# Kernel optimization log

Measured on AMD Instinct MI355X. Metric: run time of the kernel, lower is better.

The kernel has to match this reference:

```python
import jax, jax.numpy as jnp
import numpy as np

# AWLoss config (matches init_kwargs): method='fft', filter_dim=2, filter_scale=2,
# mode='reverse', reduction='sum', epsilon=1e-9 (pre-whitening), std=1e-4, eta=0, gamma=0
EPSILON = 1e-9
STD = 1e-4
DIMS = (-2, -1)          # self.dims for filter_dim=2
FS = (3, 511, 511)       # get_filter_shape([B,3,256,256]): [nc, 2H-1, 2W-1]


def pad_signal(x, shape):
    # center-pad dims 1.. of x up to `shape` (extra sample on the right).
    pads = [(0, 0)]
    for i, s in enumerate(shape):
        p1 = (s - x.shape[i + 1]) // 2
        pads.append((p1, s - x.shape[i + 1] - p1))
    return jnp.pad(x, pads)


def make_penalty(shape, std):
    # inverted multivariate gaussian on [-1,1]^d grid: 0 at center, ->1 away
    axes = [jnp.linspace(-1.0, 1.0, n) for n in shape]
    mesh = jnp.stack(jnp.meshgrid(*axes, indexing='ij'), axis=-1)  # (h, w, 2)
    d = mesh.shape[-1]
    logp = -0.5 * jnp.sum((mesh / std) ** 2, axis=-1) \
           - 0.5 * d * jnp.log(2.0 * jnp.pi * std * std)
    rv = jnp.exp(logp)
    rv = rv / jnp.max(jnp.abs(rv))
    return -rv + jnp.max(rv)  # eta=0 => no random additive term


def wienerfft(x, y, fs, prwh):
    # least-squares Wiener filter transforming x into y, via FFT
    Fx_flip = jnp.fft.fftn(jnp.flip(x, DIMS), axes=DIMS)
    Fccorr = Fx_flip * jnp.fft.fftn(y, axes=DIMS)   # cross-correlation spectrum
    Facorr = Fx_flip * jnp.fft.fftn(x, axes=DIMS)   # auto-correlation spectrum
    Fdconv = (Fccorr + prwh) / (Facorr + prwh)      # regularized deconvolution
    # irfftn crops last axis to fs[-1]//2+1 (numpy/torch semantics match)
    rolled = jnp.fft.irfftn(Fdconv, s=fs[-2:], axes=DIMS)
    # roll: int(-n/2)-1 per trailing dim (n odd => -(n//2)-1)
    shifts = tuple(-(x.shape[i] // 2) - 1 for i in range(1, x.ndim))[-2:]
    return jnp.roll(rolled, shifts, axis=DIMS)


def awloss(recon, target):
    fs = FS
    recon_p = pad_signal(recon, fs)   # [B, C, 511, 511]
    target_p = pad_signal(target, fs)
    # mode='reverse': filter transforms target into recon
    x, y = target_p, recon_p
    v = wienerfft(x, y, fs, EPSILON)                       # [B, C, 511, 511]
    vnorm = jnp.sqrt(jnp.sum(v * v, axis=DIMS, keepdims=True))
    v = v / vnorm                                          # unit-energy filter
    T = make_penalty(fs[-2:], STD)                         # (511, 511)
    f = 0.5 * jnp.sum((T * v) ** 2)                        # reduction='sum'
    return f


def setup_inputs() -> dict:
    key = jax.random.key(0)
    k1, k2 = jax.random.split(key)
    recon = jax.random.normal(k1, (16, 3, 256, 256), dtype=jnp.float32)
    target = jax.random.normal(k2, (16, 3, 256, 256), dtype=jnp.float32)
    return {"recon": recon, "target": target}


def reference(recon, target):
    return awloss(recon, target)
```

## Files before the change

### kernel.cpp

```cpp
#include <hip/hip_runtime.h>
#include <math.h>


#define NCH 48
#define PADOFF 127
#define TWO_PI_F 6.283185307179586f

typedef float f32x4 __attribute__((ext_vector_type(4)));
typedef short s16x8 __attribute__((ext_vector_type(8)));
typedef unsigned short u16;

typedef __attribute__((address_space(1))) const unsigned char* gas_p;
typedef __attribute__((address_space(3))) unsigned char* las_p;

union frag_u { u16 u[8]; s16x8 v; };

__device__ __forceinline__ u16 f2bf(float f) {
    union { float f; unsigned u; } x; x.f = f;
    unsigned r = x.u + 0x7FFFu + ((x.u >> 16) & 1u);
    return (u16)(r >> 16);
}

#define MFMA16(A, B, C) __builtin_amdgcn_mfma_f32_16x16x32_bf16(A, B, C, 0, 0, 0)

__global__ __launch_bounds__(256) void setup(u16* __restrict__ w2f,
                                             float* __restrict__ sacc) {
    __shared__ float cs[511], sn[511];
    int tid = threadIdx.x;
    for (int i = tid; i < 511; i += 256) {
        float a = -TWO_PI_F * (float)i / 511.0f;
        cs[i] = cosf(a);
        sn[i] = sinf(a);
    }
    __syncthreads();

    int i = blockIdx.x * 256 + tid;
    int j = i & 7, l = (i >> 3) & 63, kk = (i >> 9) & 7;
    int c = (i >> 12) & 1, kt = i >> 13;
    int k1 = 16 * kt + (l & 15);
    u16 v = 0;
    if (k1 < 511) {
        int n = 32 * kk + 8 * (l >> 4) + j;
        int p = (k1 * (n + PADOFF)) % 511;
        v = f2bf(c ? sn[p] : cs[p]);
    }
    w2f[i] = v;
    if (blockIdx.x == 0 && tid < 2 * NCH) sacc[tid] = 0.0f;
}

__global__ __launch_bounds__(512, 2) void stage1(const float* __restrict__ target,
                                                 const float* __restrict__ recon,
                                                 const u16* __restrict__ w2f,
                                                 u16* __restrict__ x1t,
                                                 int c0, int cc) {
    int tid = threadIdx.x;
    int w = tid >> 6, l = tid & 63;
    int lm = l & 15, lh = l >> 4;
    int tq = blockIdx.x & 3;
    int bidh = blockIdx.x >> 2;

    __shared__ u16 tw[32768];
    {
        const u16* gp = w2f + (size_t)tq * 32768;
        s16x8 tmp[8];
        #pragma unroll
        for (int i = 0; i < 8; ++i)
            tmp[i] = *(const s16x8*)(gp + (size_t)(tid + 512 * i) * 8);
        #pragma unroll
        for (int i = 0; i < 8; ++i)
            *(s16x8*)&tw[(size_t)(tid + 512 * i) * 8] = tmp[i];
    }
    __syncthreads();

    int ntasks = 16 * cc;
    int task = bidh * 8 + w;
    if (task >= ntasks) return;
    int img = task >> 3;
    int mp  = task & 7;
    int lc = img >> 1;
    int tsel = img & 1;
    const float* src = (tsel == 0 ? target : recon) + (size_t)(c0 + lc) * 65536;

    frag_u af[2][8];
    #pragma unroll
    for (int a = 0; a < 2; ++a) {
        const float* ap = src + (size_t)(32 * mp + 16 * a + lm) * 256 + 8 * lh;
        #pragma unroll
        for (int kk = 0; kk < 8; ++kk) {
            float4 v0 = *(const float4*)(ap + 32 * kk);
            float4 v1 = *(const float4*)(ap + 32 * kk + 4);
            af[a][kk].u[0] = f2bf(v0.x); af[a][kk].u[1] = f2bf(v0.y);
            af[a][kk].u[2] = f2bf(v0.z); af[a][kk].u[3] = f2bf(v0.w);
            af[a][kk].u[4] = f2bf(v1.x); af[a][kk].u[5] = f2bf(v1.y);
            af[a][kk].u[6] = f2bf(v1.z); af[a][kk].u[7] = f2bf(v1.w);
        }
    }

    u16* chdst = x1t + (size_t)(lc * 4 + tsel * 2) * 65536;

    #pragma unroll
    for (int tt = 0; tt < 4; ++tt) {
        int t = 4 * tq + tt;
        f32x4 ac0 = {0,0,0,0}, as0 = {0,0,0,0}, ac1 = {0,0,0,0}, as1 = {0,0,0,0};
        #pragma unroll
        for (int kk = 0; kk < 8; ++kk) {
            s16x8 bc = *(const s16x8*)&tw[tt * 8192 + kk * 512 + l * 8];
            s16x8 bs = *(const s16x8*)&tw[tt * 8192 + 4096 + kk * 512 + l * 8];
            ac0 = MFMA16(af[0][kk].v, bc, ac0);
            as0 = MFMA16(af[0][kk].v, bs, as0);
            ac1 = MFMA16(af[1][kk].v, bc, ac1);
            as1 = MFMA16(af[1][kk].v, bs, as1);
        }
        ushort4 o0, o1;
        o0.x = f2bf(ac0[0]); o0.y = f2bf(ac0[1]);
        o0.z = f2bf(ac0[2]); o0.w = f2bf(ac0[3]);
        o1.x = f2bf(as0[0]); o1.y = f2bf(as0[1]);
        o1.z = f2bf(as0[2]); o1.w = f2bf(as0[3]);
        size_t off = (size_t)(16 * t + lm) * 256 + 32 * mp + 4 * lh;
        *(ushort4*)(chdst + off)         = o0;
        *(ushort4*)(chdst + 65536 + off) = o1;
        o0.x = f2bf(ac1[0]); o0.y = f2bf(ac1[1]);
        o0.z = f2bf(ac1[2]); o0.w = f2bf(ac1[3]);
        o1.x = f2bf(as1[0]); o1.y = f2bf(as1[1]);
        o1.z = f2bf(as1[2]); o1.w = f2bf(as1[3]);
        *(ushort4*)(chdst + off + 16)         = o0;
        *(ushort4*)(chdst + 65536 + off + 16) = o1;
    }
}

__global__ __launch_bounds__(256, 2) void stage2(const u16* __restrict__ x1t,
                                                 const u16* __restrict__ w2f,
                                                 float* __restrict__ sacc,
                                                 int c0, int cc) {
    int tid = threadIdx.x;
    int w = tid >> 6, l = tid & 63;
    int lm = l & 15, lh = l >> 4;
    int t   = blockIdx.x & 15;
    int o   = (blockIdx.x >> 4) & 3;
    int chg = blockIdx.x >> 6;
    int ch0 = chg * 6;
    int nch = cc - ch0; if (nch > 6) nch = 6;
    if (nch <= 0) return;

    __shared__ u16 sbufA[16384];
    __shared__ u16 sbufB[16384];
    __shared__ float red[4][12];

    int kt0 = 8 * o + 2 * w;
    s16x8 twr0[8], twi0[8], twr1[8], twi1[8];
    {
        const u16* p0 = w2f + (size_t)kt0 * 8192 + l * 8;
        const u16* p1 = w2f + (size_t)(kt0 + 1) * 8192 + l * 8;
        #pragma unroll
        for (int kk = 0; kk < 8; ++kk) {
            twr0[kk] = *(const s16x8*)(p0 + kk * 512);
            twi0[kk] = *(const s16x8*)(p0 + 4096 + kk * 512);
            twr1[kk] = *(const s16x8*)(p1 + kk * 512);
            twi1[kk] = *(const s16x8*)(p1 + 4096 + kk * 512);
        }
    }

    int k2 = 16 * t + lm;
    float wgt = (k2 == 0) ? 1.f : 2.f;
    int rowoff = (16 * t + lm) * 256 + 8 * lh;
    float s1a[6] = {0,0,0,0,0,0}, s2a[6] = {0,0,0,0,0,0};

#define STAGE(BUF, LC) do {                                                   \
    const u16* cb_ = x1t + (size_t)(4 * (LC)) * 65536;                        \
    _Pragma("unroll")                                                         \
    for (int q = 0; q < 8; ++q) {                                             \
        int pair_ = w * 8 + q;                                                \
        int p_ = pair_ >> 3, kk_ = pair_ & 7;                                 \
        const u16* g_ = cb_ + (size_t)p_ * 65536 + rowoff + 32 * kk_;         \
        __builtin_amdgcn_global_load_lds((gas_p)g_,                           \
            (las_p)&BUF[pair_ * 512], 16, 0, 0);                              \
    } } while (0)

#define COMPUTE(BUF, I) do {                                                  \
    f32x4 c0rr = {0,0,0,0}, c0ii = {0,0,0,0}, c0ri = {0,0,0,0}, c0ir = {0,0,0,0}; \
    f32x4 d0rr = {0,0,0,0}, d0ii = {0,0,0,0}, d0ri = {0,0,0,0}, d0ir = {0,0,0,0}; \
    f32x4 c1rr = {0,0,0,0}, c1ii = {0,0,0,0}, c1ri = {0,0,0,0}, c1ir = {0,0,0,0}; \
    f32x4 d1rr = {0,0,0,0}, d1ii = {0,0,0,0}, d1ri = {0,0,0,0}, d1ir = {0,0,0,0}; \
    _Pragma("unroll")                                                         \
    for (int kk = 0; kk < 8; ++kk) {                                          \
        const u16* fb = &BUF[kk * 512 + l * 8];                               \
        s16x8 ar = *(const s16x8*)(fb);                                       \
        s16x8 ai = *(const s16x8*)(fb + 4096);                                \
        s16x8 br = *(const s16x8*)(fb + 8192);                                \
        s16x8 bi = *(const s16x8*)(fb + 12288);                               \
        c0rr = MFMA16(twr0[kk], ar, c0rr);                                    \
        c0ii = MFMA16(twi0[kk], ai, c0ii);                                    \
        c0ri = MFMA16(twr0[kk], ai, c0ri);                                    \
        c0ir = MFMA16(twi0[kk], ar, c0ir);                                    \
        d0rr = MFMA16(twr0[kk], br, d0rr);                                    \
        d0ii = MFMA16(twi0[kk], bi, d0ii);                                    \
        d0ri = MFMA16(twr0[kk], bi, d0ri);                                    \
        d0ir = MFMA16(twi0[kk], br, d0ir);                                    \
        c1rr = MFMA16(twr1[kk], ar, c1rr);                                    \
        c1ii = MFMA16(twi1[kk], ai, c1ii);                                    \
        c1ri = MFMA16(twr1[kk], ai, c1ri);                                    \
        c1ir = MFMA16(twi1[kk], ar, c1ir);                                    \
        d1rr = MFMA16(twr1[kk], br, d1rr);                                    \
        d1ii = MFMA16(twi1[kk], bi, d1ii);                                    \
        d1ri = MFMA16(twr1[kk], bi, d1ri);                                    \
        d1ir = MFMA16(twi1[kk], br, d1ir);                                    \
    }                                                                         \
    _Pragma("unroll")                                                         \
    for (int r = 0; r < 4; ++r) {                                             \
        {                                                                     \
            float Xr = c0rr[r] - c0ii[r], Xi = c0ri[r] + c0ir[r];             \
            float Yr = d0rr[r] - d0ii[r], Yi = d0ri[r] + d0ir[r];             \
            float Pr = Xr * Yr + Xi * Yi;                                     \
            float Pi = Xr * Yi - Xi * Yr;                                     \
            float Q  = Xr * Xr + Xi * Xi;                                     \
            float inv = 1.0f / (Q * Q + 1e-30f);                              \
            s1a[I] += wgt * Pr * Q * inv;                                     \
            s2a[I] += wgt * (Pr * Pr + Pi * Pi) * inv;                        \
        }                                                                     \
        {                                                                     \
            int k1 = 16 * (kt0 + 1) + 4 * lh + r;                             \
            float wg2 = (k1 < 511) ? wgt : 0.f;                               \
            float Xr = c1rr[r] - c1ii[r], Xi = c1ri[r] + c1ir[r];             \
            float Yr = d1rr[r] - d1ii[r], Yi = d1ri[r] + d1ir[r];             \
            float Pr = Xr * Yr + Xi * Yi;                                     \
            float Pi = Xr * Yi - Xi * Yr;                                     \
            float Q  = Xr * Xr + Xi * Xi;                                     \
            float inv = 1.0f / (Q * Q + 1e-30f);                              \
            s1a[I] += wg2 * Pr * Q * inv;                                     \
            s2a[I] += wg2 * (Pr * Pr + Pi * Pi) * inv;                        \
        }                                                                     \
    } } while (0)

    STAGE(sbufA, ch0);
    __syncthreads();

    #pragma unroll
    for (int i = 0; i < 6; i += 2) {
        if (i >= nch) break;
        if (i + 1 < nch) STAGE(sbufB, ch0 + i + 1);
        COMPUTE(sbufA, i);
        __syncthreads();
        if (i + 1 < nch) {
            if (i + 2 < nch) STAGE(sbufA, ch0 + i + 2);
            COMPUTE(sbufB, i + 1);
            __syncthreads();
        }
    }
#undef STAGE
#undef COMPUTE

    #pragma unroll
    for (int i = 0; i < 6; ++i) {
        #pragma unroll
        for (int off = 32; off > 0; off >>= 1) {
            s1a[i] += __shfl_down(s1a[i], off);
            s2a[i] += __shfl_down(s2a[i], off);
        }
    }
    if (l == 0) {
        #pragma unroll
        for (int i = 0; i < 6; ++i) {
            red[w][2 * i]     = s1a[i];
            red[w][2 * i + 1] = s2a[i];
        }
    }
    __syncthreads();
    if (tid < 12) {
        int i = tid >> 1;
        if (i < nch) {
            float v = red[0][tid] + red[1][tid] + red[2][tid] + red[3][tid];
            atomicAdd(&sacc[(tid & 1) * NCH + c0 + ch0 + i], v);
        }
    }
}

__global__ void finalize(const float* __restrict__ s, float* __restrict__ out) {
    int t = threadIdx.x;
    float v = 0.f;
    if (t < NCH) {
        float s1 = s[t], s2 = s[NCH + t];
        v = (s2 != 0.f) ? (s1 * s1) / s2 : 0.f;
    }
    for (int off = 32; off > 0; off >>= 1) v += __shfl_down(v, off);
    if (t == 0) out[0] = 24.0f - 0.5f * v / 261121.0f;
}

extern "C" void kernel_launch(void* const* d_in, const int* in_sizes, int n_in,
                              void* d_out, int out_size, void* d_ws, size_t ws_size,
                              hipStream_t stream) {
    const float* recon  = (const float*)d_in[0];
    const float* target = (const float*)d_in[1];
    float* out = (float*)d_out;
    char* ws = (char*)d_ws;

    const size_t OFF_W2F = 0;
    const size_t OFF_S   = OFF_W2F + 524288;
    const size_t OFF_X1  = OFF_S + 512;

    u16*   w2f  = (u16*)(ws + OFF_W2F);
    float* sacc = (float*)(ws + OFF_S);
    u16*   x1t  = (u16*)(ws + OFF_X1);

    const size_t perch = 4ull * 65536 * 2;
    size_t avail = (ws_size > OFF_X1) ? ws_size - OFF_X1 : 0;
    int chunk = (int)(avail / perch);
    if (chunk > NCH) chunk = NCH;
    if (chunk < 1) chunk = 1;

    setup<<<dim3(1024), dim3(256), 0, stream>>>(w2f, sacc);

    for (int c0 = 0; c0 < NCH; c0 += chunk) {
        int cc = (NCH - c0 < chunk) ? (NCH - c0) : chunk;
        int ngrp = (cc + 5) / 6;
        stage1<<<dim3(512), dim3(512), 0, stream>>>(target, recon, w2f, x1t, c0, cc);
        stage2<<<dim3(64 * ngrp), dim3(256), 0, stream>>>(x1t, w2f, sacc, c0, cc);
    }
    finalize<<<dim3(1), dim3(64), 0, stream>>>(sacc, out);
}
```

Measured before the change: 67.00 us.

## Restructure stage1 to stage input tile in LDS and keep twiddles in registers

Stage1 now gives each block a 64-row slab of one image. It converts that slab to bf16 into LDS in MFMA fragment layout, while each wave holds two twiddle column tiles in registers. Previously each block loaded a 64KB twiddle table into LDS and each wave read its input fragments directly from global memory. The new scheme cuts LDS footprint and raises reuse of the input fragments across four row sub-tiles. In exchange it increases register pressure (32 twiddle fragments plus 16 accumulators per lane), and the grid size now follows the channel chunk.

```diff
diff --git a/kernel.cpp b/kernel.cpp
--- a/kernel.cpp
+++ b/kernel.cpp
@@ -48,83 +48,101 @@
     if (blockIdx.x == 0 && tid < 2 * NCH) sacc[tid] = 0.0f;
 }
 
-__global__ __launch_bounds__(512, 2) void stage1(const float* __restrict__ target,
+__global__ __launch_bounds__(256, 2) void stage1(const float* __restrict__ target,
                                                  const float* __restrict__ recon,
                                                  const u16* __restrict__ w2f,
                                                  u16* __restrict__ x1t,
-                                                 int c0, int cc) {
+                                                 int c0) {
     int tid = threadIdx.x;
     int w = tid >> 6, l = tid & 63;
     int lm = l & 15, lh = l >> 4;
-    int tq = blockIdx.x & 3;
-    int bidh = blockIdx.x >> 2;
-
-    __shared__ u16 tw[32768];
+    int h   = blockIdx.x & 1;
+    int q   = (blockIdx.x >> 1) & 3;
+    int imgl = blockIdx.x >> 3;
+    int lc = imgl >> 1;
+    int tsel = imgl & 1;
+    const float* src = (tsel == 0 ? target : recon) + (size_t)(c0 + lc) * 65536;
+    int r0 = 64 * q;
+
+    __shared__ u16 lin[16384];
+
     {
-        const u16* gp = w2f + (size_t)tq * 32768;
-        s16x8 tmp[8];
-        #pragma unroll
-        for (int i = 0; i < 8; ++i)
-            tmp[i] = *(const s16x8*)(gp + (size_t)(tid + 512 * i) * 8);
-        #pragma unroll
-        for (int i = 0; i < 8; ++i)
-            *(s16x8*)&tw[(size_t)(tid + 512 * i) * 8] = tmp[i];
+        int row = tid >> 2;
+        int cg  = tid & 3;
+        const float* rp = src + (size_t)(r0 + row) * 256 + cg * 64;
+        float4 v[16];
+        #pragma unroll
+        for (int i = 0; i < 16; ++i) v[i] = *(const float4*)(rp + 4 * i);
+        u16 b[64];
+        #pragma unroll
+        for (int i = 0; i < 16; ++i) {
+            b[4*i]   = f2bf(v[i].x); b[4*i+1] = f2bf(v[i].y);
+            b[4*i+2] = f2bf(v[i].z); b[4*i+3] = f2bf(v[i].w);
+        }
+        int s = row >> 4, lmw = row & 15;
+        #pragma unroll
+        for (int i2 = 0; i2 < 8; ++i2) {
+            int col0 = cg * 64 + i2 * 8;
+            int kk = col0 >> 5, lhw = (col0 >> 3) & 3;
+            u16* dst = &lin[((s * 8 + kk) * 512) + (lhw * 16 + lmw) * 8];
+            *(s16x8*)dst = *(const s16x8*)&b[i2 * 8];
+        }
+    }
+
+    int t0 = 8 * h + 2 * w;
+    s16x8 tw00[8], tw01[8], tw10[8], tw11[8];
+    {
+        const u16* p0 = w2f + (size_t)t0 * 8192 + l * 8;
+        const u16* p1 = w2f + (size_t)(t0 + 1) * 8192 + l * 8;
+        #pragma unroll
+        for (int kk = 0; kk < 8; ++kk) {
+            tw00[kk] = *(const s16x8*)(p0 + kk * 512);
+            tw01[kk] = *(const s16x8*)(p0 + 4096 + kk * 512);
+            tw10[kk] = *(const s16x8*)(p1 + kk * 512);
+            tw11[kk] = *(const s16x8*)(p1 + 4096 + kk * 512);
+        }
     }
     __syncthreads();
 
-    int ntasks = 16 * cc;
-    int task = bidh * 8 + w;
-    if (task >= ntasks) return;
-    int img = task >> 3;
-    int mp  = task & 7;
-    int lc = img >> 1;
-    int tsel = img & 1;
-    const float* src = (tsel == 0 ? target : recon) + (size_t)(c0 + lc) * 65536;
-
-    frag_u af[2][8];
-    #pragma unroll
-    for (int a = 0; a < 2; ++a) {
-        const float* ap = src + (size_t)(32 * mp + 16 * a + lm) * 256 + 8 * lh;
-        #pragma unroll
-        for (int kk = 0; kk < 8; ++kk) {
-            float4 v0 = *(const float4*)(ap + 32 * kk);
-            float4 v1 = *(const float4*)(ap + 32 * kk + 4);
-            af[a][kk].u[0] = f2bf(v0.x); af[a][kk].u[1] = f2bf(v0.y);
-            af[a][kk].u[2] = f2bf(v0.z); af[a][kk].u[3] = f2bf(v0.w);
-            af[a][kk].u[4] = f2bf(v1.x); af[a][kk].u[5] = f2bf(v1.y);
-            af[a][kk].u[6] = f2bf(v1.z); af[a][kk].u[7] = f2bf(v1.w);
+    f32x4 a00[4], a01[4], a10[4], a11[4];
+    #pragma unroll
+    for (int s = 0; s < 4; ++s) {
+        a00[s] = (f32x4){0,0,0,0}; a01[s] = (f32x4){0,0,0,0};
+        a10[s] = (f32x4){0,0,0,0}; a11[s] = (f32x4){0,0,0,0};
+    }
+    #pragma unroll
+    for (int kk = 0; kk < 8; ++kk) {
+        s16x8 af[4];
+        #pragma unroll
+        for (int s = 0; s < 4; ++s)
+            af[s] = *(const s16x8*)&lin[((s * 8 + kk) * 512) + l * 8];
+        #pragma unroll
+        for (int s = 0; s < 4; ++s) {
+            a00[s] = MFMA16(af[s], tw00[kk], a00[s]);
+            a01[s] = MFMA16(af[s], tw01[kk], a01[s]);
+            a10[s] = MFMA16(af[s], tw10[kk], a10[s]);
+            a11[s] = MFMA16(af[s], tw11[kk], a11[s]);
         }
     }
 
     u16* chdst = x1t + (size_t)(lc * 4 + tsel * 2) * 65536;
-
-    #pragma unroll
-    for (int tt = 0; tt < 4; ++tt) {
-        int t = 4 * tq + tt;
-        f32x4 ac0 = {0,0,0,0}, as0 = {0,0,0,0}, ac1 = {0,0,0,0}, as1 = {0,0,0,0};
-        #pragma unroll
-        for (int kk = 0; kk < 8; ++kk) {
-            s16x8 bc = *(const s16x8*)&tw[tt * 8192 + kk * 512 + l * 8];
-            s16x8 bs = *(const s16x8*)&tw[tt * 8192 + 4096 + kk * 512 + l * 8];
-            ac0 = MFMA16(af[0][kk].v, bc, ac0);
-            as0 = MFMA16(af[0][kk].v, bs, as0);
-            ac1 = MFMA16(af[1][kk].v, bc, ac1);
-            as1 = MFMA16(af[1][kk].v, bs, as1);
-        }
-        ushort4 o0, o1;
-        o0.x = f2bf(ac0[0]); o0.y = f2bf(ac0[1]);
-        o0.z = f2bf(ac0[2]); o0.w = f2bf(ac0[3]);
-        o1.x = f2bf(as0[0]); o1.y = f2bf(as0[1]);
-        o1.z = f2bf(as0[2]); o1.w = f2bf(as0[3]);
-        size_t off = (size_t)(16 * t + lm) * 256 + 32 * mp + 4 * lh;
-        *(ushort4*)(chdst + off)         = o0;
-        *(ushort4*)(chdst + 65536 + off) = o1;
-        o0.x = f2bf(ac1[0]); o0.y = f2bf(ac1[1]);
-        o0.z = f2bf(ac1[2]); o0.w = f2bf(ac1[3]);
-        o1.x = f2bf(as1[0]); o1.y = f2bf(as1[1]);
-        o1.z = f2bf(as1[2]); o1.w = f2bf(as1[3]);
-        *(ushort4*)(chdst + off + 16)         = o0;
-        *(ushort4*)(chdst + 65536 + off + 16) = o1;
+    #pragma unroll
+    for (int s = 0; s < 4; ++s) {
+        size_t off0 = (size_t)(16 * t0 + lm) * 256 + r0 + 16 * s + 4 * lh;
+        size_t off1 = off0 + 4096;
+        ushort4 o;
+        o.x = f2bf(a00[s][0]); o.y = f2bf(a00[s][1]);
+        o.z = f2bf(a00[s][2]); o.w = f2bf(a00[s][3]);
+        *(ushort4*)(chdst + off0) = o;
+        o.x = f2bf(a01[s][0]); o.y = f2bf(a01[s][1]);
+        o.z = f2bf(a01[s][2]); o.w = f2bf(a01[s][3]);
+        *(ushort4*)(chdst + 65536 + off0) = o;
+        o.x = f2bf(a10[s][0]); o.y = f2bf(a10[s][1]);
+        o.z = f2bf(a10[s][2]); o.w = f2bf(a10[s][3]);
+        *(ushort4*)(chdst + off1) = o;
+        o.x = f2bf(a11[s][0]); o.y = f2bf(a11[s][1]);
+        o.z = f2bf(a11[s][2]); o.w = f2bf(a11[s][3]);
+        *(ushort4*)(chdst + 65536 + off1) = o;
     }
 }
 
@@ -312,7 +330,7 @@
     for (int c0 = 0; c0 < NCH; c0 += chunk) {
         int cc = (NCH - c0 < chunk) ? (NCH - c0) : chunk;
         int ngrp = (cc + 5) / 6;
-        stage1<<<dim3(512), dim3(512), 0, stream>>>(target, recon, w2f, x1t, c0, cc);
+        stage1<<<dim3(16 * cc), dim3(256), 0, stream>>>(target, recon, w2f, x1t, c0);
         stage2<<<dim3(64 * ngrp), dim3(256), 0, stream>>>(x1t, w2f, sacc, c0, cc);
     }
     finalize<<<dim3(1), dim3(64), 0, stream>>>(sacc, out);
```

Result: faster. 61.25 us (-8.6%).
